# Kernel optimization log

Measured on AMD Instinct MI355X. Metric: run time of the kernel, lower is better.

Reference implementation:

```python
import jax, jax.numpy as jnp
import numpy as np

IS_DECODER = True
NEG = -100000.0


def setup_inputs() -> dict:
    key = jax.random.key(0)
    ks = jax.random.split(key, 8)
    B, S, E, H = 8, 2048, 1024, 64
    return {
        "hidden_state": jax.random.normal(ks[0], (B, S, E), dtype=jnp.float32),
        "attention_masks": jax.random.randint(ks[1], (B, S), 0, 2, dtype=jnp.int32),
        "Wq": jax.random.normal(ks[2], (E, H), dtype=jnp.float32) / np.sqrt(E),
        "bq": jax.random.normal(ks[3], (H,), dtype=jnp.float32) * 0.02,
        "Wk": jax.random.normal(ks[4], (E, H), dtype=jnp.float32) / np.sqrt(E),
        "bk": jax.random.normal(ks[5], (H,), dtype=jnp.float32) * 0.02,
        "Wv": jax.random.normal(ks[6], (E, H), dtype=jnp.float32) / np.sqrt(E),
        "bv": jax.random.normal(ks[7], (H,), dtype=jnp.float32) * 0.02,
    }


def reference(hidden_state, attention_masks, Wq, bq, Wk, bk, Wv, bv):
    # projections: q,k,v [B,S,H]
    q = hidden_state @ Wq + bq
    k = hidden_state @ Wk + bk
    v = hidden_state @ Wv + bv
    dim = q.shape[-1]
    # scores [B,S,S]
    score = jnp.einsum("bqh,bkh->bqk", q, k) / jnp.sqrt(jnp.float32(dim))
    m = attention_masks.astype(score.dtype)  # [B,S]
    pad = 1.0 - m
    amm = m[:, :, None] * m[:, None, :]      # [B,S,S]
    pmm = pad[:, :, None] * pad[:, None, :]
    if IS_DECODER:
        S = m.shape[-1]
        amm = amm * jnp.tril(jnp.ones((S, S), dtype=score.dtype))
    coupling = 1.0 - amm - pmm
    score = score + coupling * NEG
    weights = jax.nn.softmax(score, axis=-1)
    return jnp.einsum("bqk,bkh->bqh", weights, v)
```

## Files before the change

### kernel.cpp

```cpp
#include <hip/hip_runtime.h>

typedef float f32x4 __attribute__((ext_vector_type(4)));
typedef float f32x16 __attribute__((ext_vector_type(16)));
typedef unsigned int u32x4 __attribute__((ext_vector_type(4)));
typedef __bf16 bf16x8 __attribute__((ext_vector_type(8)));
typedef unsigned short ushort_t;

#define NEG2 (-144269.5f)
#define SCLQ (0.18033688f)

constexpr int Ss = 2048, Ee = 1024, Hh = 64;

static __device__ __forceinline__ ushort_t f2bfu(float f) {
  return __builtin_bit_cast(ushort_t, (__bf16)f);
}
static __device__ __forceinline__ f32x4 mfma16(bf16x8 a, bf16x8 b, f32x4 c) {
  return __builtin_amdgcn_mfma_f32_16x16x32_bf16(a, b, c, 0, 0, 0);
}
static __device__ __forceinline__ f32x16 mfma32(bf16x8 a, bf16x8 b, f32x16 c) {
  return __builtin_amdgcn_mfma_f32_32x32x16_bf16(a, b, c, 0, 0, 0);
}
static __device__ __forceinline__ unsigned cvtpk(float a, float b) {
  unsigned r;
  asm("v_cvt_pk_bf16_f32 %0, %1, %2" : "=v"(r) : "v"(a), "v"(b));
  return r;
}
static __device__ __forceinline__ void swap32(unsigned& a, unsigned& b) {
  asm("v_permlane32_swap_b32 %0, %1" : "+v"(a), "+v"(b));
}

__global__ __launch_bounds__(256) void k_wtrans(const float* __restrict__ Wq,
                                                const float* __restrict__ Wk,
                                                const float* __restrict__ Wv,
                                                ushort_t* __restrict__ Wt) {
  __shared__ float tile[64][65];
  const float* W = (blockIdx.y == 0) ? Wq : (blockIdx.y == 1 ? Wk : Wv);
  int kt = blockIdx.x, t = threadIdx.x;
  int r = t >> 2, cq = t & 3;
  const float* src = W + (kt * 64 + r) * Hh + cq * 16;
#pragma unroll
  for (int j = 0; j < 16; j += 4) {
    float4 v = *reinterpret_cast<const float4*>(src + j);
    tile[r][cq * 16 + j + 0] = v.x;
    tile[r][cq * 16 + j + 1] = v.y;
    tile[r][cq * 16 + j + 2] = v.z;
    tile[r][cq * 16 + j + 3] = v.w;
  }
  __syncthreads();
  int n = t >> 2, kq = t & 3;
  ushort_t ob[16];
#pragma unroll
  for (int j = 0; j < 16; ++j) ob[j] = f2bfu(tile[kq * 16 + j][n]);
  ushort_t* dst = Wt + ((size_t)blockIdx.y * 64 + n) * Ee + kt * 64 + kq * 16;
  reinterpret_cast<uint4*>(dst)[0] = reinterpret_cast<uint4*>(ob)[0];
  reinterpret_cast<uint4*>(dst)[1] = reinterpret_cast<uint4*>(ob)[1];
}

__global__ __launch_bounds__(512, 4) void k_proj(const float* __restrict__ hs,
                                                 const float* __restrict__ bq,
                                                 const float* __restrict__ bk,
                                                 const float* __restrict__ bv,
                                                 const ushort_t* __restrict__ Wt,
                                                 const int* __restrict__ am,
                                                 ushort_t* __restrict__ q,
                                                 ushort_t* __restrict__ k,
                                                 ushort_t* __restrict__ vt,
                                                 float* __restrict__ pen) {
  __shared__ __align__(16) ushort_t bufA[2][64][72];
  __shared__ __align__(16) ushort_t bufW[2][192][72];

  int t = threadIdx.x, w = t >> 6, l = t & 63, g = l >> 4, c = l & 15;
  int wm = w >> 1, wn = w & 1;
  int row0 = blockIdx.x * 64;

  int ar = t >> 3, ach = t & 7;
  const float* agp = hs + (size_t)(row0 + ar) * Ee + ach * 8;
  const ushort_t* wgp = Wt + (size_t)(t >> 3) * Ee + (t & 7) * 8;

  f32x4 acc[6];
#pragma unroll
  for (int nt = 0; nt < 6; ++nt) acc[nt] = f32x4{0.f, 0.f, 0.f, 0.f};

  float4 aR0, aR1;
  u32x4 wR[3];

  auto LOAD = [&](int kk) {
    aR0 = *reinterpret_cast<const float4*>(agp + kk);
    aR1 = *reinterpret_cast<const float4*>(agp + kk + 4);
#pragma unroll
    for (int j = 0; j < 3; ++j)
      wR[j] = *reinterpret_cast<const u32x4*>(wgp + (size_t)j * 64 * Ee + kk);
  };
  auto WRITE = [&](int buf) {
    bf16x8 av;
    av[0] = (__bf16)aR0.x; av[1] = (__bf16)aR0.y; av[2] = (__bf16)aR0.z; av[3] = (__bf16)aR0.w;
    av[4] = (__bf16)aR1.x; av[5] = (__bf16)aR1.y; av[6] = (__bf16)aR1.z; av[7] = (__bf16)aR1.w;
    *reinterpret_cast<bf16x8*>(&bufA[buf][ar][ach * 8]) = av;
#pragma unroll
    for (int j = 0; j < 3; ++j)
      *reinterpret_cast<u32x4*>(&bufW[buf][(t >> 3) + j * 64][(t & 7) * 8]) = wR[j];
  };
  auto COMPUTE = [&](int buf) {
    const ushort_t* Ab = &bufA[buf][wm * 16 + c][0];
    bf16x8 af0 = *reinterpret_cast<const bf16x8*>(Ab + g * 8);
    bf16x8 af1 = *reinterpret_cast<const bf16x8*>(Ab + 32 + g * 8);
#pragma unroll
    for (int nt = 0; nt < 6; ++nt) {
      const ushort_t* Wb = &bufW[buf][wn * 96 + nt * 16 + c][0];
      bf16x8 b0 = *reinterpret_cast<const bf16x8*>(Wb + g * 8);
      bf16x8 b1 = *reinterpret_cast<const bf16x8*>(Wb + 32 + g * 8);
      acc[nt] = mfma16(af0, b0, acc[nt]);
      acc[nt] = mfma16(af1, b1, acc[nt]);
    }
  };

  LOAD(0);
  WRITE(0);
  __syncthreads();

  int cur = 0;
  for (int s = 0; s < 16; ++s) {
    if (s < 15) LOAD((s + 1) * 64);
    COMPUTE(cur);
    if (s < 15) {
      __syncthreads();
      WRITE(cur ^ 1);
      __syncthreads();
      cur ^= 1;
    }
  }

#pragma unroll
  for (int nt = 0; nt < 6; ++nt) {
    int T = wn * 6 + nt;
    int m = T >> 2;
    int h = (T & 3) * 16 + c;
    const float* bias = (m == 0) ? bq : ((m == 1) ? bk : bv);
    float bb = bias[h];
#pragma unroll
    for (int i = 0; i < 4; ++i) {
      int row = row0 + wm * 16 + g * 4 + i;
      float val = acc[nt][i] + bb;
      if (m == 0) {
        q[(size_t)row * Hh + h] = f2bfu(val * SCLQ);
      } else if (m == 1) {
        k[(size_t)row * Hh + h] = f2bfu(val);
      } else {
        int bi = row >> 11, s2 = row & 2047;
        vt[((size_t)(bi * 64 + h)) * Ss + s2] = f2bfu(val);
      }
    }
  }

  if (t < 64) {
    int grow = row0 + t;
    int bi = grow >> 11, s2 = grow & 2047;
    int mv = am[grow];
    pen[((size_t)bi * 2 + 0) * Ss + s2] = mv ? 0.f : NEG2;
    pen[((size_t)bi * 2 + 1) * Ss + s2] = mv ? NEG2 : 0.f;
  }
}

__global__ __launch_bounds__(256, 2) void k_attn(const ushort_t* __restrict__ qs,
                                                 const ushort_t* __restrict__ km,
                                                 const ushort_t* __restrict__ vt,
                                                 const int* __restrict__ am,
                                                 const float* __restrict__ pen,
                                                 float* __restrict__ out) {
  __shared__ __align__(16) char smem[65536];
  __shared__ float lls[4][32];

  int t = threadIdx.x, w = t >> 6, l = t & 63, lo = l & 31, hi = l >> 5;
  int bid = blockIdx.x;
  int b = bid & 7, q0 = (bid >> 3) * 32;

  const ushort_t* qp = qs + ((size_t)(b * Ss + q0 + lo)) * Hh + hi * 8;
  bf16x8 qf[4];
#pragma unroll
  for (int c = 0; c < 4; ++c) qf[c] = *reinterpret_cast<const bf16x8*>(qp + c * 16);

  int mq = am[b * Ss + q0 + lo];
  float negq = mq ? NEG2 : 0.f;
  const float* psel = pen + ((size_t)b * 2 + (mq ? 0 : 1)) * Ss;

  float ll = 0.f;
  f32x16 o0 = {0.f, 0.f, 0.f, 0.f, 0.f, 0.f, 0.f, 0.f, 0.f, 0.f, 0.f, 0.f, 0.f, 0.f, 0.f, 0.f};
  f32x16 o1 = o0;
  const f32x16 z16 = o0;

  const int r0 = t >> 3, c8 = t & 7;
  const int rv0 = t >> 4, cv = t & 15;
  const ushort_t* kg = km + ((size_t)b * Ss + r0) * Hh + c8 * 8;
  const ushort_t* vg = vt + ((size_t)(b * 64 + rv0)) * Ss + cv * 8;
  const int swzK = (r0 & 7) << 4;
  const int swzV = (rv0 & 7) << 4;

  u32x4 kr0, kr1, kr2, kr3, vr0, vr1, vr2, vr3;

  auto GLOAD = [&](int kv0) {
    kr0 = *reinterpret_cast<const u32x4*>(kg + (size_t)(kv0 + 0) * Hh);
    kr1 = *reinterpret_cast<const u32x4*>(kg + (size_t)(kv0 + 32) * Hh);
    kr2 = *reinterpret_cast<const u32x4*>(kg + (size_t)(kv0 + 64) * Hh);
    kr3 = *reinterpret_cast<const u32x4*>(kg + (size_t)(kv0 + 96) * Hh);
    vr0 = *reinterpret_cast<const u32x4*>(vg + (size_t)0 * Ss + kv0);
    vr1 = *reinterpret_cast<const u32x4*>(vg + (size_t)16 * Ss + kv0);
    vr2 = *reinterpret_cast<const u32x4*>(vg + (size_t)32 * Ss + kv0);
    vr3 = *reinterpret_cast<const u32x4*>(vg + (size_t)48 * Ss + kv0);
  };
  auto LWRITE = [&](int buf) {
    char* Kb = smem + buf * 16384;
    *reinterpret_cast<u32x4*>(Kb + ((((r0 + 0) * 128) + c8 * 16) ^ swzK)) = kr0;
    *reinterpret_cast<u32x4*>(Kb + ((((r0 + 32) * 128) + c8 * 16) ^ swzK)) = kr1;
    *reinterpret_cast<u32x4*>(Kb + ((((r0 + 64) * 128) + c8 * 16) ^ swzK)) = kr2;
    *reinterpret_cast<u32x4*>(Kb + ((((r0 + 96) * 128) + c8 * 16) ^ swzK)) = kr3;
    char* Vb = smem + 32768 + buf * 16384;
    *reinterpret_cast<u32x4*>(Vb + ((((rv0 + 0) * 256) + cv * 16) ^ swzV)) = vr0;
    *reinterpret_cast<u32x4*>(Vb + ((((rv0 + 16) * 256) + cv * 16) ^ swzV)) = vr1;
    *reinterpret_cast<u32x4*>(Vb + ((((rv0 + 32) * 256) + cv * 16) ^ swzV)) = vr2;
    *reinterpret_cast<u32x4*>(Vb + ((((rv0 + 48) * 256) + cv * 16) ^ swzV)) = vr3;
  };

  const int swz = (lo & 7) << 4;

  auto COMPUTE = [&](int buf, int it) {
    const char* Kb = smem + buf * 16384;
    const char* Vb = smem + 32768 + buf * 16384;
    const int kvw = it * 128 + w * 32;
    const int krow = w * 32 + lo;

    bf16x8 kf0 = *reinterpret_cast<const bf16x8*>(Kb + ((krow * 128 + 0 + hi * 16) ^ swz));
    bf16x8 kf1 = *reinterpret_cast<const bf16x8*>(Kb + ((krow * 128 + 32 + hi * 16) ^ swz));
    bf16x8 kf2 = *reinterpret_cast<const bf16x8*>(Kb + ((krow * 128 + 64 + hi * 16) ^ swz));
    bf16x8 kf3 = *reinterpret_cast<const bf16x8*>(Kb + ((krow * 128 + 96 + hi * 16) ^ swz));
    bf16x8 vf00 = *reinterpret_cast<const bf16x8*>(Vb + ((lo * 256 + w * 64 + hi * 16) ^ swz));
    bf16x8 vf10 = *reinterpret_cast<const bf16x8*>(Vb + ((lo * 256 + w * 64 + hi * 16 + 32) ^ swz));
    bf16x8 vf01 = *reinterpret_cast<const bf16x8*>(Vb + (((lo + 32) * 256 + w * 64 + hi * 16) ^ swz));
    bf16x8 vf11 = *reinterpret_cast<const bf16x8*>(Vb + (((lo + 32) * 256 + w * 64 + hi * 16 + 32) ^ swz));

    f32x4 pv[4];
#pragma unroll
    for (int j = 0; j < 4; ++j)
      pv[j] = *reinterpret_cast<const f32x4*>(psel + kvw + j * 8 + hi * 4);

    f32x16 sc = mfma32(kf0, qf[0], z16);
    sc = mfma32(kf1, qf[1], sc);
    sc = mfma32(kf2, qf[2], sc);
    sc = mfma32(kf3, qf[3], sc);

    if (kvw == q0) {
#pragma unroll
      for (int r = 0; r < 16; ++r) {
        int kr = (r & 3) + 8 * (r >> 2) + 4 * hi;
        sc[r] += pv[r >> 2][r & 3] + ((kr > lo) ? negq : 0.f);
      }
    } else {
      float addt = (kvw > q0) ? negq : 0.f;
#pragma unroll
      for (int r = 0; r < 16; ++r) sc[r] += pv[r >> 2][r & 3] + addt;
    }

    float p[16], ts = 0.f;
#pragma unroll
    for (int r = 0; r < 16; ++r) {
      p[r] = __builtin_amdgcn_exp2f(sc[r]);
      ts += p[r];
    }
    ll += ts;

    unsigned x0 = cvtpk(p[0], p[1]), y0 = cvtpk(p[2], p[3]);
    unsigned z0 = cvtpk(p[4], p[5]), w0 = cvtpk(p[6], p[7]);
    swap32(x0, z0);
    swap32(y0, w0);
    unsigned x1 = cvtpk(p[8], p[9]), y1 = cvtpk(p[10], p[11]);
    unsigned z1 = cvtpk(p[12], p[13]), w1 = cvtpk(p[14], p[15]);
    swap32(x1, z1);
    swap32(y1, w1);
    bf16x8 pa0 = __builtin_bit_cast(bf16x8, u32x4{x0, y0, z0, w0});
    bf16x8 pa1 = __builtin_bit_cast(bf16x8, u32x4{x1, y1, z1, w1});

    o0 = mfma32(pa0, vf00, o0);
    o0 = mfma32(pa1, vf10, o0);
    o1 = mfma32(pa0, vf01, o1);
    o1 = mfma32(pa1, vf11, o1);
  };

  GLOAD(0);
  LWRITE(0);
  __syncthreads();
  int cur = 0;
  for (int it = 0; it < 16; ++it) {
    if (it < 15) GLOAD((it + 1) * 128);
    COMPUTE(cur, it);
    if (it < 15) {
      __syncthreads();
      LWRITE(cur ^ 1);
      __syncthreads();
      cur ^= 1;
    }
  }

  ll += __shfl_xor(ll, 32);

  __syncthreads();
  float (*obuf)[32][68] = reinterpret_cast<float(*)[32][68]>(smem);
#pragma unroll
  for (int r = 0; r < 16; ++r) {
    int qrow = (r & 3) + 8 * (r >> 2) + 4 * hi;
    obuf[w][qrow][lo] = o0[r];
    obuf[w][qrow][32 + lo] = o1[r];
  }
  if (hi == 0) lls[w][lo] = ll;
  __syncthreads();

  int qr = t >> 3, dg = t & 7;
  float lg = 0.f;
#pragma unroll
  for (int ww = 0; ww < 4; ++ww) lg += lls[ww][qr];
  float a8[8] = {0.f, 0.f, 0.f, 0.f, 0.f, 0.f, 0.f, 0.f};
#pragma unroll
  for (int ww = 0; ww < 4; ++ww) {
    float4 c0 = *reinterpret_cast<const float4*>(&obuf[ww][qr][dg * 8]);
    float4 c1 = *reinterpret_cast<const float4*>(&obuf[ww][qr][dg * 8 + 4]);
    a8[0] += c0.x; a8[1] += c0.y; a8[2] += c0.z; a8[3] += c0.w;
    a8[4] += c1.x; a8[5] += c1.y; a8[6] += c1.z; a8[7] += c1.w;
  }
  float inv = 1.f / lg;
  float4 r0v = {a8[0] * inv, a8[1] * inv, a8[2] * inv, a8[3] * inv};
  float4 r1v = {a8[4] * inv, a8[5] * inv, a8[6] * inv, a8[7] * inv};
  float* op = out + ((size_t)(b * Ss + q0 + qr)) * Hh + dg * 8;
  *reinterpret_cast<float4*>(op) = r0v;
  *reinterpret_cast<float4*>(op + 4) = r1v;
}

extern "C" void kernel_launch(void* const* d_in, const int* in_sizes, int n_in,
                              void* d_out, int out_size, void* d_ws, size_t ws_size,
                              hipStream_t stream) {
  const float* hs = (const float*)d_in[0];
  const int* am = (const int*)d_in[1];
  const float* Wq = (const float*)d_in[2];
  const float* bq = (const float*)d_in[3];
  const float* Wk = (const float*)d_in[4];
  const float* bk = (const float*)d_in[5];
  const float* Wv = (const float*)d_in[6];
  const float* bv = (const float*)d_in[7];
  float* out = (float*)d_out;

  char* ws = (char*)d_ws;
  ushort_t* qsp = (ushort_t*)(ws + 0);
  ushort_t* kp = (ushort_t*)(ws + (2u << 20));
  ushort_t* vtp = (ushort_t*)(ws + (4u << 20));
  ushort_t* wtp = (ushort_t*)(ws + (6u << 20));
  float* penp = (float*)(ws + (6u << 20) + (512u << 10));

  k_wtrans<<<dim3(16, 3), 256, 0, stream>>>(Wq, Wk, Wv, wtp);
  k_proj<<<dim3(256), 512, 0, stream>>>(hs, bq, bk, bv, wtp, am, qsp, kp, vtp, penp);
  k_attn<<<dim3(512), 256, 0, stream>>>(qsp, kp, vtp, am, penp, out);
}
```

Baseline: 55.27 us.

## Share K/V tiles across two query groups per block and pipeline loads

```diff
diff --git a/kernel.cpp b/kernel.cpp
--- a/kernel.cpp
+++ b/kernel.cpp
@@ -161,25 +161,27 @@
   }
 }
 
-__global__ __launch_bounds__(256, 2) void k_attn(const ushort_t* __restrict__ qs,
+__global__ __launch_bounds__(512, 2) void k_attn(const ushort_t* __restrict__ qs,
                                                  const ushort_t* __restrict__ km,
                                                  const ushort_t* __restrict__ vt,
                                                  const int* __restrict__ am,
                                                  const float* __restrict__ pen,
                                                  float* __restrict__ out) {
   __shared__ __align__(16) char smem[65536];
-  __shared__ float lls[4][32];
+  __shared__ float lls[4][64];
 
   int t = threadIdx.x, w = t >> 6, l = t & 63, lo = l & 31, hi = l >> 5;
+  int wq = w >> 2, wk = w & 3;
   int bid = blockIdx.x;
-  int b = bid & 7, q0 = (bid >> 3) * 32;
-
-  const ushort_t* qp = qs + ((size_t)(b * Ss + q0 + lo)) * Hh + hi * 8;
+  int b = bid & 7, q0 = (bid >> 3) * 64;
+  int qg0 = q0 + wq * 32;
+
+  const ushort_t* qp = qs + ((size_t)(b * Ss + qg0 + lo)) * Hh + hi * 8;
   bf16x8 qf[4];
 #pragma unroll
   for (int c = 0; c < 4; ++c) qf[c] = *reinterpret_cast<const bf16x8*>(qp + c * 16);
 
-  int mq = am[b * Ss + q0 + lo];
+  int mq = am[b * Ss + qg0 + lo];
   float negq = mq ? NEG2 : 0.f;
   const float* psel = pen + ((size_t)b * 2 + (mq ? 0 : 1)) * Ss;
 
@@ -195,29 +197,21 @@
   const int swzK = (r0 & 7) << 4;
   const int swzV = (rv0 & 7) << 4;
 
-  u32x4 kr0, kr1, kr2, kr3, vr0, vr1, vr2, vr3;
+  u32x4 kr0, kr1, vr0, vr1;
 
   auto GLOAD = [&](int kv0) {
     kr0 = *reinterpret_cast<const u32x4*>(kg + (size_t)(kv0 + 0) * Hh);
-    kr1 = *reinterpret_cast<const u32x4*>(kg + (size_t)(kv0 + 32) * Hh);
-    kr2 = *reinterpret_cast<const u32x4*>(kg + (size_t)(kv0 + 64) * Hh);
-    kr3 = *reinterpret_cast<const u32x4*>(kg + (size_t)(kv0 + 96) * Hh);
-    vr0 = *reinterpret_cast<const u32x4*>(vg + (size_t)0 * Ss + kv0);
-    vr1 = *reinterpret_cast<const u32x4*>(vg + (size_t)16 * Ss + kv0);
-    vr2 = *reinterpret_cast<const u32x4*>(vg + (size_t)32 * Ss + kv0);
-    vr3 = *reinterpret_cast<const u32x4*>(vg + (size_t)48 * Ss + kv0);
+    kr1 = *reinterpret_cast<const u32x4*>(kg + (size_t)(kv0 + 64) * Hh);
+    vr0 = *reinterpret_cast<const u32x4*>(vg + kv0);
+    vr1 = *reinterpret_cast<const u32x4*>(vg + (size_t)32 * Ss + kv0);
   };
   auto LWRITE = [&](int buf) {
     char* Kb = smem + buf * 16384;
-    *reinterpret_cast<u32x4*>(Kb + ((((r0 + 0) * 128) + c8 * 16) ^ swzK)) = kr0;
-    *reinterpret_cast<u32x4*>(Kb + ((((r0 + 32) * 128) + c8 * 16) ^ swzK)) = kr1;
-    *reinterpret_cast<u32x4*>(Kb + ((((r0 + 64) * 128) + c8 * 16) ^ swzK)) = kr2;
-    *reinterpret_cast<u32x4*>(Kb + ((((r0 + 96) * 128) + c8 * 16) ^ swzK)) = kr3;
+    *reinterpret_cast<u32x4*>(Kb + (((r0 + 0) * 128 + c8 * 16) ^ swzK)) = kr0;
+    *reinterpret_cast<u32x4*>(Kb + (((r0 + 64) * 128 + c8 * 16) ^ swzK)) = kr1;
     char* Vb = smem + 32768 + buf * 16384;
-    *reinterpret_cast<u32x4*>(Vb + ((((rv0 + 0) * 256) + cv * 16) ^ swzV)) = vr0;
-    *reinterpret_cast<u32x4*>(Vb + ((((rv0 + 16) * 256) + cv * 16) ^ swzV)) = vr1;
-    *reinterpret_cast<u32x4*>(Vb + ((((rv0 + 32) * 256) + cv * 16) ^ swzV)) = vr2;
-    *reinterpret_cast<u32x4*>(Vb + ((((rv0 + 48) * 256) + cv * 16) ^ swzV)) = vr3;
+    *reinterpret_cast<u32x4*>(Vb + (((rv0 + 0) * 256 + cv * 16) ^ swzV)) = vr0;
+    *reinterpret_cast<u32x4*>(Vb + (((rv0 + 32) * 256 + cv * 16) ^ swzV)) = vr1;
   };
 
   const int swz = (lo & 7) << 4;
@@ -225,17 +219,17 @@
   auto COMPUTE = [&](int buf, int it) {
     const char* Kb = smem + buf * 16384;
     const char* Vb = smem + 32768 + buf * 16384;
-    const int kvw = it * 128 + w * 32;
-    const int krow = w * 32 + lo;
+    const int kvw = it * 128 + wk * 32;
+    const int krow = wk * 32 + lo;
 
     bf16x8 kf0 = *reinterpret_cast<const bf16x8*>(Kb + ((krow * 128 + 0 + hi * 16) ^ swz));
     bf16x8 kf1 = *reinterpret_cast<const bf16x8*>(Kb + ((krow * 128 + 32 + hi * 16) ^ swz));
     bf16x8 kf2 = *reinterpret_cast<const bf16x8*>(Kb + ((krow * 128 + 64 + hi * 16) ^ swz));
     bf16x8 kf3 = *reinterpret_cast<const bf16x8*>(Kb + ((krow * 128 + 96 + hi * 16) ^ swz));
-    bf16x8 vf00 = *reinterpret_cast<const bf16x8*>(Vb + ((lo * 256 + w * 64 + hi * 16) ^ swz));
-    bf16x8 vf10 = *reinterpret_cast<const bf16x8*>(Vb + ((lo * 256 + w * 64 + hi * 16 + 32) ^ swz));
-    bf16x8 vf01 = *reinterpret_cast<const bf16x8*>(Vb + (((lo + 32) * 256 + w * 64 + hi * 16) ^ swz));
-    bf16x8 vf11 = *reinterpret_cast<const bf16x8*>(Vb + (((lo + 32) * 256 + w * 64 + hi * 16 + 32) ^ swz));
+    bf16x8 vf00 = *reinterpret_cast<const bf16x8*>(Vb + ((lo * 256 + wk * 64 + hi * 16) ^ swz));
+    bf16x8 vf10 = *reinterpret_cast<const bf16x8*>(Vb + ((lo * 256 + wk * 64 + hi * 16 + 32) ^ swz));
+    bf16x8 vf01 = *reinterpret_cast<const bf16x8*>(Vb + (((lo + 32) * 256 + wk * 64 + hi * 16) ^ swz));
+    bf16x8 vf11 = *reinterpret_cast<const bf16x8*>(Vb + (((lo + 32) * 256 + wk * 64 + hi * 16 + 32) ^ swz));
 
     f32x4 pv[4];
 #pragma unroll
@@ -247,14 +241,14 @@
     sc = mfma32(kf2, qf[2], sc);
     sc = mfma32(kf3, qf[3], sc);
 
-    if (kvw == q0) {
+    if (kvw == qg0) {
 #pragma unroll
       for (int r = 0; r < 16; ++r) {
         int kr = (r & 3) + 8 * (r >> 2) + 4 * hi;
         sc[r] += pv[r >> 2][r & 3] + ((kr > lo) ? negq : 0.f);
       }
     } else {
-      float addt = (kvw > q0) ? negq : 0.f;
+      float addt = (kvw > qg0) ? negq : 0.f;
 #pragma unroll
       for (int r = 0; r < 16; ++r) sc[r] += pv[r >> 2][r & 3] + addt;
     }
@@ -286,36 +280,31 @@
 
   GLOAD(0);
   LWRITE(0);
-  __syncthreads();
+  GLOAD(128);
   int cur = 0;
   for (int it = 0; it < 16; ++it) {
-    if (it < 15) GLOAD((it + 1) * 128);
+    __syncthreads();
+    if (it < 15) LWRITE(cur ^ 1);
+    if (it < 14) GLOAD((it + 2) * 128);
     COMPUTE(cur, it);
-    if (it < 15) {
-      __syncthreads();
-      LWRITE(cur ^ 1);
-      __syncthreads();
-      cur ^= 1;
-    }
+    cur ^= 1;
   }
 
   ll += __shfl_xor(ll, 32);
 
   __syncthreads();
-  float (*obuf)[32][68] = reinterpret_cast<float(*)[32][68]>(smem);
+  float (*obuf)[64][64] = reinterpret_cast<float(*)[64][64]>(smem);
 #pragma unroll
   for (int r = 0; r < 16; ++r) {
     int qrow = (r & 3) + 8 * (r >> 2) + 4 * hi;
-    obuf[w][qrow][lo] = o0[r];
-    obuf[w][qrow][32 + lo] = o1[r];
-  }
-  if (hi == 0) lls[w][lo] = ll;
+    obuf[wk][wq * 32 + qrow][lo] = o0[r];
+    obuf[wk][wq * 32 + qrow][32 + lo] = o1[r];
+  }
+  if (hi == 0) lls[wk][wq * 32 + lo] = ll;
   __syncthreads();
 
   int qr = t >> 3, dg = t & 7;
-  float lg = 0.f;
-#pragma unroll
-  for (int ww = 0; ww < 4; ++ww) lg += lls[ww][qr];
+  float lg = lls[0][qr] + lls[1][qr] + lls[2][qr] + lls[3][qr];
   float a8[8] = {0.f, 0.f, 0.f, 0.f, 0.f, 0.f, 0.f, 0.f};
 #pragma unroll
   for (int ww = 0; ww < 4; ++ww) {
@@ -354,5 +343,5 @@
 
   k_wtrans<<<dim3(16, 3), 256, 0, stream>>>(Wq, Wk, Wv, wtp);
   k_proj<<<dim3(256), 512, 0, stream>>>(hs, bq, bk, bv, wtp, am, qsp, kp, vtp, penp);
-  k_attn<<<dim3(512), 256, 0, stream>>>(qsp, kp, vtp, am, penp, out);
-}
+  k_attn<<<dim3(256), 512, 0, stream>>>(qsp, kp, vtp, am, penp, out);
+}
```

Result: no change. 54.46 us (-1.5%).
